# Optimization experiments

Measured on AMD Instinct MI355X. Metric: run time of the kernel, lower is better.

Reference implementation:

```python
import jax, jax.numpy as jnp
import numpy as np

B, LT, LI, D, H, K = 32, 512, 576, 768, 8, 512


def setup_inputs() -> dict:
    key = jax.random.key(0)
    ks = jax.random.split(key, 10)
    s = 0.02
    return {
        "text_hidden_states": jax.random.normal(ks[0], (B, LT, D), jnp.float32),
        "image_hidden_states": jax.random.normal(ks[1], (B, LI, D), jnp.float32),
        "text_mask": jnp.ones((B, LT), jnp.int32),
        "Wb": jax.random.normal(ks[2], (H, D, D), jnp.float32) * s,   # per-head Linear weights [out,in]
        "Wv": jax.random.normal(ks[3], (K, D), jnp.float32) * s,
        "Wq": jax.random.normal(ks[4], (K, D), jnp.float32) * s,
        "Whv": jax.random.normal(ks[5], (K,), jnp.float32) * s,
        "Whq": jax.random.normal(ks[6], (K,), jnp.float32) * s,
        "Wo": jax.random.normal(ks[7], (D, D * H), jnp.float32) * s,  # output_proj weight [out,in]
        "bo": jnp.zeros((D,), jnp.float32),
    }


def reference(text_hidden_states, image_hidden_states, text_mask, Wb, Wv, Wq, Whv, Whq, Wo, bo):
    text, image = text_hidden_states, image_hidden_states
    # per-head text projection (torch Linear: x @ W.T), batched over heads
    pt = jnp.einsum('bxe,hfe->hbxf', text, Wb)                 # [H,B,LT,D]
    aff = jnp.einsum('hbxe,bye->hbxy', pt, image)              # [H,B,LT,LI]
    wv_v = jnp.einsum('bye,ke->byk', image, Wv)                # [B,LI,K] (head-shared)
    wq_q = jnp.einsum('bxe,ke->bxk', text, Wq)                 # [B,LT,K]
    wqqc = jnp.einsum('bxk,hbxy->hbyk', wq_q, aff)             # [H,B,LI,K]
    wvvc = jnp.einsum('byk,hbxy->hbxk', wv_v, aff)             # [H,B,LT,K]
    h_v = jnp.tanh(wv_v[None] + wqqc)
    h_q = jnp.tanh(wq_q[None] + wvvc)
    att_v = jax.nn.softmax(jnp.einsum('hbyk,k->hby', h_v, Whv), axis=-1)  # over image tokens
    att_q = jax.nn.softmax(jnp.einsum('hbxk,k->hbx', h_q, Whq), axis=-1)  # over text tokens
    ctx_v = jnp.einsum('hby,byd->hbd', att_v, image)
    ctx_q = jnp.einsum('hbx,bxd->hbd', att_q, text)
    head_out = ctx_v + ctx_q                                   # [H,B,D]
    combined = jnp.transpose(head_out, (1, 0, 2)).reshape(text.shape[0], -1)  # [B,H*D]
    return combined @ Wo.T + bo
```

## Files before the change

kernel.cpp:

```cpp
#include <hip/hip_runtime.h>
#include <math.h>

#define B_  32
#define LT_ 512
#define LI_ 576
#define LIP 640
#define D_  768
#define H_  8
#define K_  512
#define NTOK  (LI_ + LT_)
#define CSPLIT 16
#define TPB   (NTOK / CSPLIT)
#define NHEAD ((long)H_ * B_ * D_)

typedef __attribute__((ext_vector_type(4))) short short4v;
typedef __attribute__((ext_vector_type(8))) unsigned short ushort8;
typedef __attribute__((ext_vector_type(8))) _Float16 f16x8;
typedef __attribute__((ext_vector_type(4))) float f32x4;

__device__ __forceinline__ unsigned short f2h(float x) {
  _Float16 h = (_Float16)x;
  return __builtin_bit_cast(unsigned short, h);
}
__device__ __forceinline__ float h2f(unsigned short u) {
  return (float)__builtin_bit_cast(_Float16, u);
}
__device__ __forceinline__ float ftanh(float x) {
  float e = __expf(2.f * x);
  return 1.f - 2.f * __builtin_amdgcn_rcpf(e + 1.f);
}

__device__ __forceinline__ void gl_lds16(const void* g, void* l) {
  __builtin_amdgcn_global_load_lds(
      (const __attribute__((address_space(1))) void*)g,
      (__attribute__((address_space(3))) void*)l, 16, 0, 0);
}

#define EPI_PLAIN 0
#define EPI_T     1
#define EPI_TANH  2

template<int EPI>
__global__ __launch_bounds__(256) void mfma_nt(
    const unsigned short* __restrict__ Ag, const unsigned short* __restrict__ Bg,
    unsigned short* __restrict__ Cg, unsigned short* __restrict__ CTg,
    int Kd, int gx, int gy,
    long sA, long sB, long sC, long sCT,
    const unsigned short* __restrict__ baseg, long sBase,
    const float* __restrict__ wvec, float* __restrict__ outv, int valid_rows)
{
  const int orig = blockIdx.x, nwg = gridDim.x;
  const int q = nwg >> 3, r = nwg & 7;
  const int xcd = orig & 7, idx = orig >> 3;
  const int wg = (xcd < r ? xcd * (q + 1) : r * (q + 1) + (xcd - r) * q) + idx;
  const int bx = wg % gx, tmp = wg / gx, by = tmp % gy, bz = tmp / gy;

  __shared__ unsigned short LDSU[EPI == EPI_T ? 17408 : 16384];
  unsigned short* As = LDSU;
  unsigned short* Bs = LDSU + 8192;

  const int t = threadIdx.x;
  const int lane = t & 63, w = t >> 6;
  const int wr = w >> 1, wc = w & 1;
  const int m0 = bx * 128, n0 = by * 128;
  const int ldc = gy << 7;
  const unsigned short* A  = Ag + (long)bz * sA;
  const unsigned short* Bm = Bg + (long)bz * sB;

  const int srow = w * 8 + (lane >> 3);
  const unsigned short *aP0, *aP1, *aP2, *aP3, *bP0, *bP1, *bP2, *bP3;
  {
    int r0 = srow, r1 = srow + 32, r2 = srow + 64, r3 = srow + 96;
    int c0 = ((lane & 7) ^ (r0 & 7)) * 8, c1 = ((lane & 7) ^ (r1 & 7)) * 8;
    int c2 = ((lane & 7) ^ (r2 & 7)) * 8, c3 = ((lane & 7) ^ (r3 & 7)) * 8;
    aP0 = A + (long)(m0 + r0) * Kd + c0;  bP0 = Bm + (long)(n0 + r0) * Kd + c0;
    aP1 = A + (long)(m0 + r1) * Kd + c1;  bP1 = Bm + (long)(n0 + r1) * Kd + c1;
    aP2 = A + (long)(m0 + r2) * Kd + c2;  bP2 = Bm + (long)(n0 + r2) * Kd + c2;
    aP3 = A + (long)(m0 + r3) * Kd + c3;  bP3 = Bm + (long)(n0 + r3) * Kd + c3;
  }
  unsigned short* asb0 = As + (w * 8) * 64;
  unsigned short* asb1 = As + (32 + w * 8) * 64;
  unsigned short* asb2 = As + (64 + w * 8) * 64;
  unsigned short* asb3 = As + (96 + w * 8) * 64;
  unsigned short* bsb0 = Bs + (w * 8) * 64;
  unsigned short* bsb1 = Bs + (32 + w * 8) * 64;
  unsigned short* bsb2 = Bs + (64 + w * 8) * 64;
  unsigned short* bsb3 = Bs + (96 + w * 8) * 64;

  f32x4 acc[4][4];
  #pragma unroll
  for (int i = 0; i < 4; ++i)
    #pragma unroll
    for (int j = 0; j < 4; ++j)
      acc[i][j] = (f32x4){0.f, 0.f, 0.f, 0.f};

  const int rl = lane & 15, g = lane >> 4;
  const int aslot = (g ^ (rl & 7)) << 3;
  const int aslot2 = aslot ^ 32;

  for (int k0 = 0; k0 < Kd; k0 += 64) {
    __syncthreads();
    gl_lds16(aP0 + k0, asb0);  gl_lds16(bP0 + k0, bsb0);
    gl_lds16(aP1 + k0, asb1);  gl_lds16(bP1 + k0, bsb1);
    gl_lds16(aP2 + k0, asb2);  gl_lds16(bP2 + k0, bsb2);
    gl_lds16(aP3 + k0, asb3);  gl_lds16(bP3 + k0, bsb3);
    __syncthreads();
    f16x8 af[4], bf[4];
    #pragma unroll
    for (int i = 0; i < 4; ++i) {
      af[i] = *(const f16x8*)&As[(wr * 64 + i * 16 + rl) * 64 + aslot];
      bf[i] = *(const f16x8*)&Bs[(wc * 64 + i * 16 + rl) * 64 + aslot];
    }
    #pragma unroll
    for (int i = 0; i < 4; ++i)
      #pragma unroll
      for (int j = 0; j < 4; ++j)
        acc[i][j] = __builtin_amdgcn_mfma_f32_16x16x32_f16(af[i], bf[j], acc[i][j], 0, 0, 0);
    #pragma unroll
    for (int i = 0; i < 4; ++i) {
      af[i] = *(const f16x8*)&As[(wr * 64 + i * 16 + rl) * 64 + aslot2];
      bf[i] = *(const f16x8*)&Bs[(wc * 64 + i * 16 + rl) * 64 + aslot2];
    }
    #pragma unroll
    for (int i = 0; i < 4; ++i)
      #pragma unroll
      for (int j = 0; j < 4; ++j)
        acc[i][j] = __builtin_amdgcn_mfma_f32_16x16x32_f16(af[i], bf[j], acc[i][j], 0, 0, 0);
  }

  const int rg = lane >> 4;
  if (EPI != EPI_TANH) {
    unsigned short* C = Cg + (long)bz * sC;
    unsigned short* T = LDSU;
    if (EPI == EPI_T) __syncthreads();
    #pragma unroll
    for (int i = 0; i < 4; ++i)
      #pragma unroll
      for (int j = 0; j < 4; ++j) {
        unsigned short hv[4];
        #pragma unroll
        for (int rr = 0; rr < 4; ++rr) {
          int row = wr * 64 + i * 16 + rg * 4 + rr;
          int col = wc * 64 + j * 16 + rl;
          hv[rr] = f2h(acc[i][j][rr]);
          C[(long)(m0 + row) * ldc + n0 + col] = hv[rr];
        }
        if (EPI == EPI_T) {
          int col = wc * 64 + j * 16 + rl;
          int row0 = wr * 64 + i * 16 + rg * 4;
          *(short4v*)&T[col * 136 + row0] =
              (short4v){(short)hv[0], (short)hv[1], (short)hv[2], (short)hv[3]};
        }
      }
    if (EPI == EPI_T) {
      __syncthreads();
      unsigned short* CT = CTg + (long)bz * sCT;
      const int ldTm = gx << 7;
      #pragma unroll
      for (int rr = 0; rr < 8; ++rr) {
        int rn = rr * 16 + (t >> 4);
        int c8 = (t & 15) * 8;
        *(ushort8*)(CT + (long)(n0 + rn) * ldTm + m0 + c8) = *(const ushort8*)&T[rn * 136 + c8];
      }
    }
  } else {
    const unsigned short* base = baseg + (long)bz * sBase;
    float* outp = outv + (long)bz * valid_rows;
    #pragma unroll
    for (int i = 0; i < 4; ++i)
      #pragma unroll
      for (int rr = 0; rr < 4; ++rr) {
        int row = m0 + wr * 64 + i * 16 + rg * 4 + rr;
        float s = 0.f;
        #pragma unroll
        for (int j = 0; j < 4; ++j) {
          int col = n0 + wc * 64 + j * 16 + rl;
          float v = acc[i][rr < 0 ? 0 : j][rr] + h2f(base[(long)row * ldc + col]);
          s += ftanh(v) * wvec[col];
        }
        s += __shfl_xor(s, 1, 64);
        s += __shfl_xor(s, 2, 64);
        s += __shfl_xor(s, 4, 64);
        s += __shfl_xor(s, 8, 64);
        if (rl == 0 && row < valid_rows)
          atomicAdd(&outp[row], s);
      }
  }
}

__global__ __launch_bounds__(256) void cast_f16(
    const float* __restrict__ in, unsigned short* __restrict__ out, long n8)
{
  long i = (long)blockIdx.x * 256 + threadIdx.x;
  if (i >= n8) return;
  float4 v0 = ((const float4*)in)[i * 2];
  float4 v1 = ((const float4*)in)[i * 2 + 1];
  ushort8 o;
  o[0] = f2h(v0.x); o[1] = f2h(v0.y); o[2] = f2h(v0.z); o[3] = f2h(v0.w);
  o[4] = f2h(v1.x); o[5] = f2h(v1.y); o[6] = f2h(v1.z); o[7] = f2h(v1.w);
  *(ushort8*)(out + i * 8) = o;
}

__global__ __launch_bounds__(256) void cast_pad_image(
    const float* __restrict__ in, unsigned short* __restrict__ out)
{
  long tid = (long)blockIdx.x * 256 + threadIdx.x;
  const long tot = (long)B_ * LIP * (D_ / 8);
  if (tid >= tot) return;
  int e8 = (int)(tid % (D_ / 8));
  long rw = tid / (D_ / 8);
  int y  = (int)(rw % LIP);
  long b = rw / LIP;
  ushort8 o;
  if (y < LI_) {
    const float* p = in + ((b * LI_ + y) * D_ + e8 * 8);
    float4 v0 = *(const float4*)p, v1 = *(const float4*)(p + 4);
    o[0] = f2h(v0.x); o[1] = f2h(v0.y); o[2] = f2h(v0.z); o[3] = f2h(v0.w);
    o[4] = f2h(v1.x); o[5] = f2h(v1.y); o[6] = f2h(v1.z); o[7] = f2h(v1.w);
  } else {
    #pragma unroll
    for (int j = 0; j < 8; ++j) o[j] = 0;
  }
  *(ushort8*)(out + rw * D_ + e8 * 8) = o;
}

__global__ __launch_bounds__(256) void zero_f32(float* __restrict__ p, long n) {
  long i = (long)blockIdx.x * 256 + threadIdx.x;
  if (i < n) p[i] = 0.f;
}

__global__ __launch_bounds__(256) void softmax_att(
    const float* __restrict__ lv, const float* __restrict__ lq,
    float* __restrict__ attvG, float* __restrict__ attqG)
{
  const int b = blockIdx.x, h = blockIdx.y;
  const int t = threadIdx.x;
  __shared__ float buf[LI_];
  __shared__ float red[4];

  const float* lvp = lv + ((long)h * B_ + b) * LI_;
  float m = -1e30f;
  for (int i = t; i < LI_; i += 256) m = fmaxf(m, lvp[i]);
  #pragma unroll
  for (int o = 32; o > 0; o >>= 1) m = fmaxf(m, __shfl_down(m, o, 64));
  if ((t & 63) == 0) red[t >> 6] = m;
  __syncthreads();
  m = fmaxf(fmaxf(red[0], red[1]), fmaxf(red[2], red[3]));
  __syncthreads();
  float s = 0.f;
  for (int i = t; i < LI_; i += 256) { float e = __expf(lvp[i] - m); buf[i] = e; s += e; }
  #pragma unroll
  for (int o = 32; o > 0; o >>= 1) s += __shfl_down(s, o, 64);
  if ((t & 63) == 0) red[t >> 6] = s;
  __syncthreads();
  s = red[0] + red[1] + red[2] + red[3];
  {
    float inv = 1.f / s;
    float* op = attvG + ((long)h * B_ + b) * LI_;
    for (int i = t; i < LI_; i += 256) op[i] = buf[i] * inv;
  }
  __syncthreads();

  const float* lqp = lq + ((long)h * B_ + b) * LT_;
  m = -1e30f;
  for (int i = t; i < LT_; i += 256) m = fmaxf(m, lqp[i]);
  #pragma unroll
  for (int o = 32; o > 0; o >>= 1) m = fmaxf(m, __shfl_down(m, o, 64));
  if ((t & 63) == 0) red[t >> 6] = m;
  __syncthreads();
  m = fmaxf(fmaxf(red[0], red[1]), fmaxf(red[2], red[3]));
  __syncthreads();
  s = 0.f;
  for (int i = t; i < LT_; i += 256) { float e = __expf(lqp[i] - m); buf[i] = e; s += e; }
  #pragma unroll
  for (int o = 32; o > 0; o >>= 1) s += __shfl_down(s, o, 64);
  if ((t & 63) == 0) red[t >> 6] = s;
  __syncthreads();
  s = red[0] + red[1] + red[2] + red[3];
  {
    float inv = 1.f / s;
    float* op = attqG + ((long)h * B_ + b) * LT_;
    for (int i = t; i < LT_; i += 256) op[i] = buf[i] * inv;
  }
}

__global__ __launch_bounds__(256) void ctx_part(
    const float* __restrict__ attvG, const float* __restrict__ attqG,
    const unsigned short* __restrict__ text_h,
    float* __restrict__ head_part)
{
  const int b = blockIdx.x, d0 = blockIdx.y * 128, s = blockIdx.z;
  const int t = threadIdx.x, dl = t & 127, g = t >> 7;
  const long IMG_OFF = (long)B_ * LT_ * D_;
  __shared__ float wts[H_][TPB];
  __shared__ long  roff[TPB];
  __shared__ float red[H_][128];
  const int tok0 = s * TPB;
  for (int i = t; i < H_ * TPB; i += 256) {
    int h = i / TPB, j = i % TPB, tok = tok0 + j;
    wts[h][j] = tok < LI_ ? attvG[((long)h * B_ + b) * LI_ + tok]
                          : attqG[((long)h * B_ + b) * LT_ + (tok - LI_)];
  }
  if (t < TPB) {
    int tok = tok0 + t;
    roff[t] = tok < LI_ ? IMG_OFF + ((long)b * LIP + tok) * D_
                        : ((long)b * LT_ + (tok - LI_)) * D_;
  }
  __syncthreads();
  float acc[H_];
  #pragma unroll
  for (int h = 0; h < H_; ++h) acc[h] = 0.f;
  #pragma unroll 4
  for (int j = g; j < TPB; j += 2) {
    float val = h2f(text_h[roff[j] + d0 + dl]);
    #pragma unroll
    for (int h = 0; h < H_; ++h) acc[h] = fmaf(wts[h][j], val, acc[h]);
  }
  if (g == 1) {
    #pragma unroll
    for (int h = 0; h < H_; ++h) red[h][dl] = acc[h];
  }
  __syncthreads();
  if (g == 0) {
    float* hp = head_part + (long)s * NHEAD;
    #pragma unroll
    for (int h = 0; h < H_; ++h)
      hp[((long)h * B_ + b) * D_ + d0 + dl] = acc[h] + red[h][dl];
  }
}

__global__ __launch_bounds__(256) void reduce_head(
    const float* __restrict__ head_part, float* __restrict__ head)
{
  long i = (long)blockIdx.x * 256 + threadIdx.x;
  float s = 0.f;
  #pragma unroll
  for (int p = 0; p < CSPLIT; ++p) s += head_part[(long)p * NHEAD + i];
  head[i] = s;
}

__global__ __launch_bounds__(256) void out_proj(
    const float* __restrict__ head, const float* __restrict__ Wo,
    const float* __restrict__ bo, float* __restrict__ out)
{
  const int d = blockIdx.x, t = threadIdx.x;
  float acc[B_];
  #pragma unroll
  for (int b = 0; b < B_; ++b) acc[b] = 0.f;
  const float4* wrow4 = (const float4*)(Wo + (long)d * (H_ * D_));
  for (int k4 = t; k4 < H_ * D_ / 4; k4 += 256) {
    float4 wv = wrow4[k4];
    int k = k4 * 4;
    int h = k / D_, e = k - h * D_;
    const float* hp = head + (long)h * B_ * D_ + e;
    #pragma unroll
    for (int b = 0; b < B_; ++b) {
      const float* p = hp + (long)b * D_;
      acc[b] += wv.x * p[0] + wv.y * p[1] + wv.z * p[2] + wv.w * p[3];
    }
  }
  __shared__ float red[4][B_];
  const int w4 = t >> 6;
  #pragma unroll
  for (int b = 0; b < B_; ++b) {
    float v = acc[b];
    #pragma unroll
    for (int o = 32; o > 0; o >>= 1) v += __shfl_down(v, o, 64);
    if ((t & 63) == 0) red[w4][b] = v;
  }
  __syncthreads();
  if (t < B_)
    out[(long)t * D_ + d] = red[0][t] + red[1][t] + red[2][t] + red[3][t] + bo[d];
}

extern "C" void kernel_launch(void* const* d_in, const int* in_sizes, int n_in,
                              void* d_out, int out_size, void* d_ws, size_t ws_size,
                              hipStream_t stream)
{
  const float* text  = (const float*)d_in[0];
  const float* image = (const float*)d_in[1];
  const float* Wb  = (const float*)d_in[3];
  const float* Wv  = (const float*)d_in[4];
  const float* Wq  = (const float*)d_in[5];
  const float* Whv = (const float*)d_in[6];
  const float* Whq = (const float*)d_in[7];
  const float* Wo  = (const float*)d_in[8];
  const float* bo  = (const float*)d_in[9];
  float* out = (float*)d_out;

  const long N_TEXT = (long)B_ * LT_ * D_;
  const long N_IMGP = (long)B_ * LIP * D_;
  const long N_WV   = (long)K_ * D_;
  const long N_WB   = (long)H_ * D_ * D_;
  const long N_WVV  = (long)B_ * LIP * K_;
  const long N_WQQ  = (long)B_ * LT_ * K_;
  const long N_PT   = (long)B_ * LT_ * D_;
  const long N_AFF  = (long)B_ * LT_ * LIP;
  const long N_LV   = (long)H_ * B_ * LI_;
  const long N_LQ   = (long)H_ * B_ * LT_;

  unsigned short* wsu = (unsigned short*)d_ws;
  long off = 0;
  unsigned short* text_h  = wsu + off; off += N_TEXT;
  unsigned short* image_p = wsu + off; off += N_IMGP;
  unsigned short* Wv_h    = wsu + off; off += N_WV;
  unsigned short* Wq_h    = wsu + off; off += N_WV;
  unsigned short* Wb_h    = wsu + off; off += N_WB;
  unsigned short* wv_v    = wsu + off; off += N_WVV;
  unsigned short* wq_q    = wsu + off; off += N_WQQ;
  unsigned short* wv_vT   = wsu + off; off += N_WVV;
  unsigned short* wq_qT   = wsu + off; off += N_WQQ;
  unsigned short* pt_h    = wsu + off; off += N_PT;
  unsigned short* aff     = wsu + off; off += N_AFF;
  unsigned short* affT    = wsu + off; off += N_AFF;
  float* lv        = (float*)(wsu + off);
  float* lq        = lv + N_LV;
  float* attvG     = lq + N_LQ;
  float* attqG     = attvG + N_LV;
  float* head      = attqG + N_LQ;
  float* head_part = head + NHEAD;
  const size_t need = (size_t)off * 2 +
      (size_t)(2 * (N_LV + N_LQ) + NHEAD + CSPLIT * NHEAD) * 4;
  if (ws_size < need) return;

  dim3 blk(256);

  cast_f16<<<(unsigned)(N_TEXT / 8 / 256), blk, 0, stream>>>(text, text_h, N_TEXT / 8);
  cast_pad_image<<<(unsigned)((B_ * LIP * (D_ / 8) + 255) / 256), blk, 0, stream>>>(image, image_p);
  cast_f16<<<(unsigned)(N_WV / 8 / 256), blk, 0, stream>>>(Wv, Wv_h, N_WV / 8);
  cast_f16<<<(unsigned)(N_WV / 8 / 256), blk, 0, stream>>>(Wq, Wq_h, N_WV / 8);
  cast_f16<<<(unsigned)(N_WB / 8 / 256), blk, 0, stream>>>(Wb, Wb_h, N_WB / 8);
  zero_f32<<<(unsigned)((N_LV + N_LQ + 255) / 256), blk, 0, stream>>>(lv, N_LV + N_LQ);

  mfma_nt<EPI_T><<<5 * 4 * B_, blk, 0, stream>>>(
      image_p, Wv_h, wv_v, wv_vT, D_, 5, 4,
      (long)LIP * D_, 0, (long)LIP * K_, (long)K_ * LIP,
      nullptr, 0, nullptr, nullptr, 0);
  mfma_nt<EPI_T><<<4 * 4 * B_, blk, 0, stream>>>(
      text_h, Wq_h, wq_q, wq_qT, D_, 4, 4,
      (long)LT_ * D_, 0, (long)LT_ * K_, (long)K_ * LT_,
      nullptr, 0, nullptr, nullptr, 0);

  for (int h = 0; h < H_; ++h) {
    mfma_nt<EPI_PLAIN><<<128 * 6, blk, 0, stream>>>(
        text_h, Wb_h + (long)h * D_ * D_, pt_h, nullptr, D_, 128, 6,
        0, 0, 0, 0, nullptr, 0, nullptr, nullptr, 0);
    mfma_nt<EPI_T><<<4 * 5 * B_, blk, 0, stream>>>(
        pt_h, image_p, aff, affT, D_, 4, 5,
        (long)LT_ * D_, (long)LIP * D_, (long)LT_ * LIP, (long)LIP * LT_,
        nullptr, 0, nullptr, nullptr, 0);
    mfma_nt<EPI_TANH><<<5 * 4 * B_, blk, 0, stream>>>(
        affT, wq_qT, nullptr, nullptr, LT_, 5, 4,
        (long)LIP * LT_, (long)K_ * LT_, 0, 0,
        wv_v, (long)LIP * K_, Whv, lv + (long)h * B_ * LI_, LI_);
    mfma_nt<EPI_TANH><<<4 * 4 * B_, blk, 0, stream>>>(
        aff, wv_vT, nullptr, nullptr, LIP, 4, 4,
        (long)LT_ * LIP, (long)K_ * LIP, 0, 0,
        wq_q, (long)LT_ * K_, Whq, lq + (long)h * B_ * LT_, LT_);
  }

  softmax_att<<<dim3(B_, H_), blk, 0, stream>>>(lv, lq, attvG, attqG);
  ctx_part<<<dim3(B_, D_ / 128, CSPLIT), blk, 0, stream>>>(attvG, attqG, text_h, head_part);
  reduce_head<<<(unsigned)(NHEAD / 256), blk, 0, stream>>>(head_part, head);
  out_proj<<<D_, blk, 0, stream>>>(head, Wo, bo, out);
}
```

Before: 1.036 ms.

## Merge GEMMs into a segmented MFMA kernel with larger tiles and an MFMA output projection

Replaces the templated 128x128 GEMM with one segmented kernel whose 256x128 tiles can hold up to three independent GEMMs per launch. The next head's text projection is overlapped with the current head's tanh-score GEMMs, and the two initial projections are launched together with the first head's projection. The casts are merged into one launch, CSPLIT is halved, and the scalar FP32 output projection becomes an f16 MFMA split-K that adds into a bias-initialised output with atomics. Larger tiles raise register pressure, row clamping adds redundant loads on padded edges, and the f16 Wo adds rounding error.

```diff
diff --git a/kernel.cpp b/kernel.cpp
--- a/kernel.cpp
+++ b/kernel.cpp
@@ -9,7 +9,7 @@
 #define H_  8
 #define K_  512
 #define NTOK  (LI_ + LT_)
-#define CSPLIT 16
+#define CSPLIT 8
 #define TPB   (NTOK / CSPLIT)
 #define NHEAD ((long)H_ * B_ * D_)
 
@@ -39,166 +39,206 @@
 #define EPI_PLAIN 0
 #define EPI_T     1
 #define EPI_TANH  2
-
-template<int EPI>
-__global__ __launch_bounds__(256) void mfma_nt(
-    const unsigned short* __restrict__ Ag, const unsigned short* __restrict__ Bg,
-    unsigned short* __restrict__ Cg, unsigned short* __restrict__ CTg,
-    int Kd, int gx, int gy,
-    long sA, long sB, long sC, long sCT,
-    const unsigned short* __restrict__ baseg, long sBase,
-    const float* __restrict__ wvec, float* __restrict__ outv, int valid_rows)
+#define EPI_OUT   3
+
+struct Seg {
+  const unsigned short *A, *B;
+  unsigned short *C, *CT;
+  const unsigned short* base;
+  const float* wvec;
+  float* outv;
+  long sA, sB, sC, sCT, sBase;
+  int Kd, lda, ldb;
+  int gx, gy, nblk, epi, Mlim, valid, ldc, ldt;
+};
+struct Params { Seg s0, s1, s2; };
+
+__global__ __launch_bounds__(256, 2) void mfma_seg(Params p)
 {
   const int orig = blockIdx.x, nwg = gridDim.x;
-  const int q = nwg >> 3, r = nwg & 7;
+  const int q8 = nwg >> 3, r8 = nwg & 7;
   const int xcd = orig & 7, idx = orig >> 3;
-  const int wg = (xcd < r ? xcd * (q + 1) : r * (q + 1) + (xcd - r) * q) + idx;
-  const int bx = wg % gx, tmp = wg / gx, by = tmp % gy, bz = tmp / gy;
-
-  __shared__ unsigned short LDSU[EPI == EPI_T ? 17408 : 16384];
+  const int wg = (xcd < r8 ? xcd * (q8 + 1) : r8 * (q8 + 1) + (xcd - r8) * q8) + idx;
+
+  Seg sg; int local;
+  if (wg < p.s0.nblk)                      { sg = p.s0; local = wg; }
+  else if (wg < p.s0.nblk + p.s1.nblk)     { sg = p.s1; local = wg - p.s0.nblk; }
+  else                                     { sg = p.s2; local = wg - p.s0.nblk - p.s1.nblk; }
+
+  const int bx = local % sg.gx;
+  const int tmp2 = local / sg.gx;
+  const int by = tmp2 % sg.gy, bz = tmp2 / sg.gy;
+
+  __shared__ unsigned short LDSU[24576];
   unsigned short* As = LDSU;
-  unsigned short* Bs = LDSU + 8192;
-
-  const int t = threadIdx.x;
-  const int lane = t & 63, w = t >> 6;
+  unsigned short* Bs = LDSU + 16384;
+
+  const int t = threadIdx.x, lane = t & 63, w = t >> 6;
   const int wr = w >> 1, wc = w & 1;
-  const int m0 = bx * 128, n0 = by * 128;
-  const int ldc = gy << 7;
-  const unsigned short* A  = Ag + (long)bz * sA;
-  const unsigned short* Bm = Bg + (long)bz * sB;
-
-  const int srow = w * 8 + (lane >> 3);
-  const unsigned short *aP0, *aP1, *aP2, *aP3, *bP0, *bP1, *bP2, *bP3;
-  {
-    int r0 = srow, r1 = srow + 32, r2 = srow + 64, r3 = srow + 96;
-    int c0 = ((lane & 7) ^ (r0 & 7)) * 8, c1 = ((lane & 7) ^ (r1 & 7)) * 8;
-    int c2 = ((lane & 7) ^ (r2 & 7)) * 8, c3 = ((lane & 7) ^ (r3 & 7)) * 8;
-    aP0 = A + (long)(m0 + r0) * Kd + c0;  bP0 = Bm + (long)(n0 + r0) * Kd + c0;
-    aP1 = A + (long)(m0 + r1) * Kd + c1;  bP1 = Bm + (long)(n0 + r1) * Kd + c1;
-    aP2 = A + (long)(m0 + r2) * Kd + c2;  bP2 = Bm + (long)(n0 + r2) * Kd + c2;
-    aP3 = A + (long)(m0 + r3) * Kd + c3;  bP3 = Bm + (long)(n0 + r3) * Kd + c3;
-  }
-  unsigned short* asb0 = As + (w * 8) * 64;
-  unsigned short* asb1 = As + (32 + w * 8) * 64;
-  unsigned short* asb2 = As + (64 + w * 8) * 64;
-  unsigned short* asb3 = As + (96 + w * 8) * 64;
-  unsigned short* bsb0 = Bs + (w * 8) * 64;
-  unsigned short* bsb1 = Bs + (32 + w * 8) * 64;
-  unsigned short* bsb2 = Bs + (64 + w * 8) * 64;
-  unsigned short* bsb3 = Bs + (96 + w * 8) * 64;
-
-  f32x4 acc[4][4];
-  #pragma unroll
-  for (int i = 0; i < 4; ++i)
+  const int m0 = bx * 256, n0 = by * 128;
+  const int Kd = sg.Kd, lda = sg.lda, ldb = sg.ldb, ldc = sg.ldc;
+  const unsigned short* A  = sg.A + (long)bz * sg.sA;
+  const unsigned short* Bm = sg.B + (long)bz * sg.sB;
+
+  const int rowb = w * 8 + (lane >> 3);
+  const int cswz = ((lane & 7) ^ (rowb & 7)) * 8;
+  const bool clampA = (m0 + 256 > sg.Mlim);
+  const unsigned short* aSrc = A  + (long)(m0 + rowb) * lda + cswz;
+  const unsigned short* bSrc = Bm + (long)(n0 + rowb) * ldb + cswz;
+  unsigned short* aDst = As + rowb * 64;
+  unsigned short* bDst = Bs + rowb * 64;
+
+  f32x4 acc[8][4];
+  #pragma unroll
+  for (int i = 0; i < 8; ++i)
     #pragma unroll
     for (int j = 0; j < 4; ++j)
       acc[i][j] = (f32x4){0.f, 0.f, 0.f, 0.f};
 
   const int rl = lane & 15, g = lane >> 4;
-  const int aslot = (g ^ (rl & 7)) << 3;
-  const int aslot2 = aslot ^ 32;
 
   for (int k0 = 0; k0 < Kd; k0 += 64) {
     __syncthreads();
-    gl_lds16(aP0 + k0, asb0);  gl_lds16(bP0 + k0, bsb0);
-    gl_lds16(aP1 + k0, asb1);  gl_lds16(bP1 + k0, bsb1);
-    gl_lds16(aP2 + k0, asb2);  gl_lds16(bP2 + k0, bsb2);
-    gl_lds16(aP3 + k0, asb3);  gl_lds16(bP3 + k0, bsb3);
+    if (!clampA) {
+      #pragma unroll
+      for (int q = 0; q < 8; ++q)
+        gl_lds16(aSrc + (long)q * 32 * lda + k0, aDst + q * 2048);
+    } else {
+      #pragma unroll
+      for (int q = 0; q < 8; ++q) {
+        int rgl = m0 + q * 32 + rowb;
+        if (rgl >= sg.Mlim) rgl = sg.Mlim - 1;
+        gl_lds16(A + (long)rgl * lda + cswz + k0, aDst + q * 2048);
+      }
+    }
+    #pragma unroll
+    for (int q = 0; q < 4; ++q)
+      gl_lds16(bSrc + (long)q * 32 * ldb + k0, bDst + q * 2048);
     __syncthreads();
-    f16x8 af[4], bf[4];
-    #pragma unroll
-    for (int i = 0; i < 4; ++i) {
-      af[i] = *(const f16x8*)&As[(wr * 64 + i * 16 + rl) * 64 + aslot];
-      bf[i] = *(const f16x8*)&Bs[(wc * 64 + i * 16 + rl) * 64 + aslot];
+
+    #pragma unroll
+    for (int h2 = 0; h2 < 2; ++h2) {
+      const int slot = (((h2 << 2) | g) ^ (rl & 7)) << 3;
+      f16x8 af[8], bf[4];
+      #pragma unroll
+      for (int i = 0; i < 8; ++i)
+        af[i] = *(const f16x8*)&As[(wr * 128 + i * 16 + rl) * 64 + slot];
+      #pragma unroll
+      for (int j = 0; j < 4; ++j)
+        bf[j] = *(const f16x8*)&Bs[(wc * 64 + j * 16 + rl) * 64 + slot];
+      #pragma unroll
+      for (int i = 0; i < 8; ++i)
+        #pragma unroll
+        for (int j = 0; j < 4; ++j)
+          acc[i][j] = __builtin_amdgcn_mfma_f32_16x16x32_f16(af[i], bf[j], acc[i][j], 0, 0, 0);
     }
-    #pragma unroll
-    for (int i = 0; i < 4; ++i)
+  }
+
+  const int rg = lane >> 4;
+  if (sg.epi <= EPI_T) {
+    unsigned short* C = sg.C + (long)bz * sg.sC;
+    #pragma unroll
+    for (int i = 0; i < 8; ++i)
       #pragma unroll
       for (int j = 0; j < 4; ++j)
-        acc[i][j] = __builtin_amdgcn_mfma_f32_16x16x32_f16(af[i], bf[j], acc[i][j], 0, 0, 0);
-    #pragma unroll
-    for (int i = 0; i < 4; ++i) {
-      af[i] = *(const f16x8*)&As[(wr * 64 + i * 16 + rl) * 64 + aslot2];
-      bf[i] = *(const f16x8*)&Bs[(wc * 64 + i * 16 + rl) * 64 + aslot2];
-    }
-    #pragma unroll
-    for (int i = 0; i < 4; ++i)
-      #pragma unroll
-      for (int j = 0; j < 4; ++j)
-        acc[i][j] = __builtin_amdgcn_mfma_f32_16x16x32_f16(af[i], bf[j], acc[i][j], 0, 0, 0);
-  }
-
-  const int rg = lane >> 4;
-  if (EPI != EPI_TANH) {
-    unsigned short* C = Cg + (long)bz * sC;
-    unsigned short* T = LDSU;
-    if (EPI == EPI_T) __syncthreads();
-    #pragma unroll
-    for (int i = 0; i < 4; ++i)
-      #pragma unroll
-      for (int j = 0; j < 4; ++j) {
-        unsigned short hv[4];
         #pragma unroll
         for (int rr = 0; rr < 4; ++rr) {
-          int row = wr * 64 + i * 16 + rg * 4 + rr;
-          int col = wc * 64 + j * 16 + rl;
-          hv[rr] = f2h(acc[i][j][rr]);
-          C[(long)(m0 + row) * ldc + n0 + col] = hv[rr];
+          int ml = wr * 128 + i * 16 + rg * 4 + rr;
+          int nl = wc * 64 + j * 16 + rl;
+          if (m0 + ml < sg.Mlim)
+            C[(long)(m0 + ml) * ldc + n0 + nl] = f2h(acc[i][j][rr]);
         }
-        if (EPI == EPI_T) {
-          int col = wc * 64 + j * 16 + rl;
-          int row0 = wr * 64 + i * 16 + rg * 4;
-          *(short4v*)&T[col * 136 + row0] =
-              (short4v){(short)hv[0], (short)hv[1], (short)hv[2], (short)hv[3]};
+    if (sg.epi == EPI_T) {
+      unsigned short* CT = sg.CT + (long)bz * sg.sCT;
+      __syncthreads();
+      #pragma unroll
+      for (int pp = 0; pp < 2; ++pp) {
+        if (wr == pp) {
+          #pragma unroll
+          for (int i = 0; i < 8; ++i)
+            #pragma unroll
+            for (int j = 0; j < 4; ++j) {
+              int nl = wc * 64 + j * 16 + rl;
+              int mh = i * 16 + rg * 4;
+              *(short4v*)&LDSU[nl * 136 + mh] = (short4v){
+                  (short)f2h(acc[i][j][0]), (short)f2h(acc[i][j][1]),
+                  (short)f2h(acc[i][j][2]), (short)f2h(acc[i][j][3])};
+            }
+        }
+        __syncthreads();
+        #pragma unroll
+        for (int rr = 0; rr < 8; ++rr) {
+          int rn = rr * 16 + (t >> 4);
+          int m8 = (t & 15) * 8;
+          int mg = m0 + pp * 128 + m8;
+          if (mg < sg.Mlim)
+            *(ushort8*)(CT + (long)(n0 + rn) * sg.ldt + mg) =
+                *(const ushort8*)&LDSU[rn * 136 + m8];
+        }
+        __syncthreads();
+      }
+    }
+  } else if (sg.epi == EPI_TANH) {
+    const unsigned short* base = sg.base + (long)bz * sg.sBase;
+    float* outp = sg.outv + (long)bz * sg.valid;
+    #pragma unroll
+    for (int i = 0; i < 8; ++i)
+      #pragma unroll
+      for (int rr = 0; rr < 4; ++rr) {
+        int row = m0 + wr * 128 + i * 16 + rg * 4 + rr;
+        if (row < sg.Mlim) {
+          float s = 0.f;
+          #pragma unroll
+          for (int j = 0; j < 4; ++j) {
+            int col = n0 + wc * 64 + j * 16 + rl;
+            float v = acc[i][j][rr] + h2f(base[(long)row * ldc + col]);
+            s += ftanh(v) * sg.wvec[col];
+          }
+          s += __shfl_xor(s, 1, 64);
+          s += __shfl_xor(s, 2, 64);
+          s += __shfl_xor(s, 4, 64);
+          s += __shfl_xor(s, 8, 64);
+          if (rl == 0 && row < sg.valid)
+            atomicAdd(&outp[row], s);
         }
       }
-    if (EPI == EPI_T) {
-      __syncthreads();
-      unsigned short* CT = CTg + (long)bz * sCT;
-      const int ldTm = gx << 7;
-      #pragma unroll
-      for (int rr = 0; rr < 8; ++rr) {
-        int rn = rr * 16 + (t >> 4);
-        int c8 = (t & 15) * 8;
-        *(ushort8*)(CT + (long)(n0 + rn) * ldTm + m0 + c8) = *(const ushort8*)&T[rn * 136 + c8];
-      }
+  } else {
+    float* outp = sg.outv;
+    if (wr == 0) {
+      #pragma unroll
+      for (int i = 0; i < 2; ++i)
+        #pragma unroll
+        for (int rr = 0; rr < 4; ++rr) {
+          int row = i * 16 + rg * 4 + rr;
+          #pragma unroll
+          for (int j = 0; j < 4; ++j) {
+            int col = n0 + wc * 64 + j * 16 + rl;
+            atomicAdd(&outp[(long)row * ldc + col], acc[i][j][rr]);
+          }
+        }
     }
-  } else {
-    const unsigned short* base = baseg + (long)bz * sBase;
-    float* outp = outv + (long)bz * valid_rows;
-    #pragma unroll
-    for (int i = 0; i < 4; ++i)
-      #pragma unroll
-      for (int rr = 0; rr < 4; ++rr) {
-        int row = m0 + wr * 64 + i * 16 + rg * 4 + rr;
-        float s = 0.f;
-        #pragma unroll
-        for (int j = 0; j < 4; ++j) {
-          int col = n0 + wc * 64 + j * 16 + rl;
-          float v = acc[i][rr < 0 ? 0 : j][rr] + h2f(base[(long)row * ldc + col]);
-          s += ftanh(v) * wvec[col];
-        }
-        s += __shfl_xor(s, 1, 64);
-        s += __shfl_xor(s, 2, 64);
-        s += __shfl_xor(s, 4, 64);
-        s += __shfl_xor(s, 8, 64);
-        if (rl == 0 && row < valid_rows)
-          atomicAdd(&outp[row], s);
-      }
-  }
-}
-
-__global__ __launch_bounds__(256) void cast_f16(
-    const float* __restrict__ in, unsigned short* __restrict__ out, long n8)
+  }
+}
+
+struct CSeg { const float* src; unsigned short* dst; long n8; };
+
+__global__ __launch_bounds__(256) void cast_multi(
+    CSeg c0, CSeg c1, CSeg c2, CSeg c3, CSeg c4)
 {
   long i = (long)blockIdx.x * 256 + threadIdx.x;
-  if (i >= n8) return;
-  float4 v0 = ((const float4*)in)[i * 2];
-  float4 v1 = ((const float4*)in)[i * 2 + 1];
+  const float* src; unsigned short* dst;
+  if      (i < c0.n8)                 { src = c0.src; dst = c0.dst; }
+  else if ((i -= c0.n8) < c1.n8)      { src = c1.src; dst = c1.dst; }
+  else if ((i -= c1.n8) < c2.n8)      { src = c2.src; dst = c2.dst; }
+  else if ((i -= c2.n8) < c3.n8)      { src = c3.src; dst = c3.dst; }
+  else if ((i -= c3.n8) < c4.n8)      { src = c4.src; dst = c4.dst; }
+  else return;
+  float4 v0 = ((const float4*)src)[i * 2];
+  float4 v1 = ((const float4*)src)[i * 2 + 1];
   ushort8 o;
   o[0] = f2h(v0.x); o[1] = f2h(v0.y); o[2] = f2h(v0.z); o[3] = f2h(v0.w);
   o[4] = f2h(v1.x); o[5] = f2h(v1.y); o[6] = f2h(v1.z); o[7] = f2h(v1.w);
-  *(ushort8*)(out + i * 8) = o;
+  *(ushort8*)(dst + i * 8) = o;
 }
 
 __global__ __launch_bounds__(256) void cast_pad_image(
@@ -229,6 +269,13 @@
   if (i < n) p[i] = 0.f;
 }
 
+__global__ __launch_bounds__(256) void init_out(
+    const float* __restrict__ bo, float* __restrict__ out)
+{
+  int i = blockIdx.x * 256 + threadIdx.x;
+  out[i] = bo[i % D_];
+}
+
 __global__ __launch_bounds__(256) void softmax_att(
     const float* __restrict__ lv, const float* __restrict__ lq,
     float* __restrict__ attvG, float* __restrict__ attqG)
@@ -330,47 +377,16 @@
 }
 
 __global__ __launch_bounds__(256) void reduce_head(
-    const float* __restrict__ head_part, float* __restrict__ head)
+    const float* __restrict__ head_part, unsigned short* __restrict__ head16)
 {
   long i = (long)blockIdx.x * 256 + threadIdx.x;
   float s = 0.f;
   #pragma unroll
   for (int p = 0; p < CSPLIT; ++p) s += head_part[(long)p * NHEAD + i];
-  head[i] = s;
-}
-
-__global__ __launch_bounds__(256) void out_proj(
-    const float* __restrict__ head, const float* __restrict__ Wo,
-    const float* __restrict__ bo, float* __restrict__ out)
-{
-  const int d = blockIdx.x, t = threadIdx.x;
-  float acc[B_];
-  #pragma unroll
-  for (int b = 0; b < B_; ++b) acc[b] = 0.f;
-  const float4* wrow4 = (const float4*)(Wo + (long)d * (H_ * D_));
-  for (int k4 = t; k4 < H_ * D_ / 4; k4 += 256) {
-    float4 wv = wrow4[k4];
-    int k = k4 * 4;
-    int h = k / D_, e = k - h * D_;
-    const float* hp = head + (long)h * B_ * D_ + e;
-    #pragma unroll
-    for (int b = 0; b < B_; ++b) {
-      const float* p = hp + (long)b * D_;
-      acc[b] += wv.x * p[0] + wv.y * p[1] + wv.z * p[2] + wv.w * p[3];
-    }
-  }
-  __shared__ float red[4][B_];
-  const int w4 = t >> 6;
-  #pragma unroll
-  for (int b = 0; b < B_; ++b) {
-    float v = acc[b];
-    #pragma unroll
-    for (int o = 32; o > 0; o >>= 1) v += __shfl_down(v, o, 64);
-    if ((t & 63) == 0) red[w4][b] = v;
-  }
-  __syncthreads();
-  if (t < B_)
-    out[(long)t * D_ + d] = red[0][t] + red[1][t] + red[2][t] + red[3][t] + bo[d];
+  int d = (int)(i % D_);
+  long hb = i / D_;
+  int b = (int)(hb % B_), h = (int)(hb / B_);
+  head16[(long)b * (H_ * D_) + (long)h * D_ + d] = f2h(s);
 }
 
 extern "C" void kernel_launch(void* const* d_in, const int* in_sizes, int n_in,
@@ -392,12 +408,14 @@
   const long N_IMGP = (long)B_ * LIP * D_;
   const long N_WV   = (long)K_ * D_;
   const long N_WB   = (long)H_ * D_ * D_;
+  const long N_WO   = (long)D_ * H_ * D_;
   const long N_WVV  = (long)B_ * LIP * K_;
   const long N_WQQ  = (long)B_ * LT_ * K_;
   const long N_PT   = (long)B_ * LT_ * D_;
   const long N_AFF  = (long)B_ * LT_ * LIP;
   const long N_LV   = (long)H_ * B_ * LI_;
   const long N_LQ   = (long)H_ * B_ * LT_;
+  const long N_H16  = (long)B_ * H_ * D_;
 
   unsigned short* wsu = (unsigned short*)d_ws;
   long off = 0;
@@ -406,6 +424,7 @@
   unsigned short* Wv_h    = wsu + off; off += N_WV;
   unsigned short* Wq_h    = wsu + off; off += N_WV;
   unsigned short* Wb_h    = wsu + off; off += N_WB;
+  unsigned short* Wo_h    = wsu + off; off += N_WO;
   unsigned short* wv_v    = wsu + off; off += N_WVV;
   unsigned short* wq_q    = wsu + off; off += N_WQQ;
   unsigned short* wv_vT   = wsu + off; off += N_WVV;
@@ -413,54 +432,104 @@
   unsigned short* pt_h    = wsu + off; off += N_PT;
   unsigned short* aff     = wsu + off; off += N_AFF;
   unsigned short* affT    = wsu + off; off += N_AFF;
+  unsigned short* head16  = wsu + off; off += N_H16;
   float* lv        = (float*)(wsu + off);
   float* lq        = lv + N_LV;
   float* attvG     = lq + N_LQ;
   float* attqG     = attvG + N_LV;
-  float* head      = attqG + N_LQ;
-  float* head_part = head + NHEAD;
+  float* head_part = attqG + N_LQ;
   const size_t need = (size_t)off * 2 +
-      (size_t)(2 * (N_LV + N_LQ) + NHEAD + CSPLIT * NHEAD) * 4;
+      (size_t)(2 * (N_LV + N_LQ) + CSPLIT * NHEAD) * 4;
   if (ws_size < need) return;
 
   dim3 blk(256);
 
-  cast_f16<<<(unsigned)(N_TEXT / 8 / 256), blk, 0, stream>>>(text, text_h, N_TEXT / 8);
+  {
+    CSeg c0{text, text_h, N_TEXT / 8};
+    CSeg c1{Wv,   Wv_h,   N_WV / 8};
+    CSeg c2{Wq,   Wq_h,   N_WV / 8};
+    CSeg c3{Wb,   Wb_h,   N_WB / 8};
+    CSeg c4{Wo,   Wo_h,   N_WO / 8};
+    long tot8 = c0.n8 + c1.n8 + c2.n8 + c3.n8 + c4.n8;
+    cast_multi<<<(unsigned)((tot8 + 255) / 256), blk, 0, stream>>>(c0, c1, c2, c3, c4);
+  }
   cast_pad_image<<<(unsigned)((B_ * LIP * (D_ / 8) + 255) / 256), blk, 0, stream>>>(image, image_p);
-  cast_f16<<<(unsigned)(N_WV / 8 / 256), blk, 0, stream>>>(Wv, Wv_h, N_WV / 8);
-  cast_f16<<<(unsigned)(N_WV / 8 / 256), blk, 0, stream>>>(Wq, Wq_h, N_WV / 8);
-  cast_f16<<<(unsigned)(N_WB / 8 / 256), blk, 0, stream>>>(Wb, Wb_h, N_WB / 8);
   zero_f32<<<(unsigned)((N_LV + N_LQ + 255) / 256), blk, 0, stream>>>(lv, N_LV + N_LQ);
-
-  mfma_nt<EPI_T><<<5 * 4 * B_, blk, 0, stream>>>(
-      image_p, Wv_h, wv_v, wv_vT, D_, 5, 4,
-      (long)LIP * D_, 0, (long)LIP * K_, (long)K_ * LIP,
-      nullptr, 0, nullptr, nullptr, 0);
-  mfma_nt<EPI_T><<<4 * 4 * B_, blk, 0, stream>>>(
-      text_h, Wq_h, wq_q, wq_qT, D_, 4, 4,
-      (long)LT_ * D_, 0, (long)LT_ * K_, (long)K_ * LT_,
-      nullptr, 0, nullptr, nullptr, 0);
+  init_out<<<(unsigned)(B_ * D_ / 256), blk, 0, stream>>>(bo, out);
+
+  Seg zs{};  zs.nblk = 0;
+
+  {
+    Seg s0{}; s0.A = image_p; s0.B = Wv_h; s0.C = wv_v; s0.CT = wv_vT;
+    s0.sA = (long)LIP * D_; s0.sC = (long)LIP * K_; s0.sCT = (long)K_ * LIP;
+    s0.Kd = D_; s0.lda = D_; s0.ldb = D_;
+    s0.gx = 3; s0.gy = 4; s0.nblk = 3 * 4 * B_; s0.epi = EPI_T;
+    s0.Mlim = LIP; s0.ldc = K_; s0.ldt = LIP;
+
+    Seg s1{}; s1.A = text_h; s1.B = Wq_h; s1.C = wq_q; s1.CT = wq_qT;
+    s1.sA = (long)LT_ * D_; s1.sC = (long)LT_ * K_; s1.sCT = (long)K_ * LT_;
+    s1.Kd = D_; s1.lda = D_; s1.ldb = D_;
+    s1.gx = 2; s1.gy = 4; s1.nblk = 2 * 4 * B_; s1.epi = EPI_T;
+    s1.Mlim = LT_; s1.ldc = K_; s1.ldt = LT_;
+
+    Seg s2{}; s2.A = text_h; s2.B = Wb_h; s2.C = pt_h;
+    s2.Kd = D_; s2.lda = D_; s2.ldb = D_;
+    s2.gx = 64; s2.gy = 6; s2.nblk = 64 * 6; s2.epi = EPI_PLAIN;
+    s2.Mlim = B_ * LT_; s2.ldc = D_;
+
+    Params P{s0, s1, s2};
+    mfma_seg<<<s0.nblk + s1.nblk + s2.nblk, blk, 0, stream>>>(P);
+  }
 
   for (int h = 0; h < H_; ++h) {
-    mfma_nt<EPI_PLAIN><<<128 * 6, blk, 0, stream>>>(
-        text_h, Wb_h + (long)h * D_ * D_, pt_h, nullptr, D_, 128, 6,
-        0, 0, 0, 0, nullptr, 0, nullptr, nullptr, 0);
-    mfma_nt<EPI_T><<<4 * 5 * B_, blk, 0, stream>>>(
-        pt_h, image_p, aff, affT, D_, 4, 5,
-        (long)LT_ * D_, (long)LIP * D_, (long)LT_ * LIP, (long)LIP * LT_,
-        nullptr, 0, nullptr, nullptr, 0);
-    mfma_nt<EPI_TANH><<<5 * 4 * B_, blk, 0, stream>>>(
-        affT, wq_qT, nullptr, nullptr, LT_, 5, 4,
-        (long)LIP * LT_, (long)K_ * LT_, 0, 0,
-        wv_v, (long)LIP * K_, Whv, lv + (long)h * B_ * LI_, LI_);
-    mfma_nt<EPI_TANH><<<4 * 4 * B_, blk, 0, stream>>>(
-        aff, wv_vT, nullptr, nullptr, LIP, 4, 4,
-        (long)LT_ * LIP, (long)K_ * LIP, 0, 0,
-        wq_q, (long)LT_ * K_, Whq, lq + (long)h * B_ * LT_, LT_);
+    {
+      Seg s0{}; s0.A = pt_h; s0.B = image_p; s0.C = aff; s0.CT = affT;
+      s0.sA = (long)LT_ * D_; s0.sB = (long)LIP * D_;
+      s0.sC = (long)LT_ * LIP; s0.sCT = (long)LIP * LT_;
+      s0.Kd = D_; s0.lda = D_; s0.ldb = D_;
+      s0.gx = 2; s0.gy = 5; s0.nblk = 2 * 5 * B_; s0.epi = EPI_T;
+      s0.Mlim = LT_; s0.ldc = LIP; s0.ldt = LT_;
+      Params P{s0, zs, zs};
+      mfma_seg<<<s0.nblk, blk, 0, stream>>>(P);
+    }
+    {
+      Seg s0{}; s0.A = affT; s0.B = wq_qT;
+      s0.base = wv_v; s0.wvec = Whv; s0.outv = lv + (long)h * B_ * LI_;
+      s0.sA = (long)LIP * LT_; s0.sB = (long)K_ * LT_; s0.sBase = (long)LIP * K_;
+      s0.Kd = LT_; s0.lda = LT_; s0.ldb = LT_;
+      s0.gx = 3; s0.gy = 4; s0.nblk = 3 * 4 * B_; s0.epi = EPI_TANH;
+      s0.Mlim = LIP; s0.valid = LI_; s0.ldc = K_;
+
+      Seg s1{}; s1.A = aff; s1.B = wv_vT;
+      s1.base = wq_q; s1.wvec = Whq; s1.outv = lq + (long)h * B_ * LT_;
+      s1.sA = (long)LT_ * LIP; s1.sB = (long)K_ * LIP; s1.sBase = (long)LT_ * K_;
+      s1.Kd = LIP; s1.lda = LIP; s1.ldb = LIP;
+      s1.gx = 2; s1.gy = 4; s1.nblk = 2 * 4 * B_; s1.epi = EPI_TANH;
+      s1.Mlim = LT_; s1.valid = LT_; s1.ldc = K_;
+
+      Seg s2 = zs;
+      if (h < H_ - 1) {
+        s2.A = text_h; s2.B = Wb_h + (long)(h + 1) * D_ * D_; s2.C = pt_h;
+        s2.Kd = D_; s2.lda = D_; s2.ldb = D_;
+        s2.gx = 64; s2.gy = 6; s2.nblk = 64 * 6; s2.epi = EPI_PLAIN;
+        s2.Mlim = B_ * LT_; s2.ldc = D_;
+      }
+      Params P{s0, s1, s2};
+      mfma_seg<<<s0.nblk + s1.nblk + s2.nblk, blk, 0, stream>>>(P);
+    }
   }
 
   softmax_att<<<dim3(B_, H_), blk, 0, stream>>>(lv, lq, attvG, attqG);
   ctx_part<<<dim3(B_, D_ / 128, CSPLIT), blk, 0, stream>>>(attvG, attqG, text_h, head_part);
-  reduce_head<<<(unsigned)(NHEAD / 256), blk, 0, stream>>>(head_part, head);
-  out_proj<<<D_, blk, 0, stream>>>(head, Wo, bo, out);
-}
+  reduce_head<<<(unsigned)(NHEAD / 256), blk, 0, stream>>>(head_part, head16);
+
+  {
+    Seg s0{}; s0.A = head16; s0.B = Wo_h; s0.outv = out;
+    s0.sA = (long)(H_ * D_ / 8); s0.sB = (long)(H_ * D_ / 8);
+    s0.Kd = H_ * D_ / 8; s0.lda = H_ * D_; s0.ldb = H_ * D_;
+    s0.gx = 1; s0.gy = 6; s0.nblk = 1 * 6 * 8; s0.epi = EPI_OUT;
+    s0.Mlim = B_; s0.valid = B_; s0.ldc = D_;
+    Params P{s0, zs, zs};
+    mfma_seg<<<s0.nblk, blk, 0, stream>>>(P);
+  }
+}
```

Result: no change. 1.037 ms (+0.0%).
